# Optimization experiments

Hardware: AMD Instinct MI355X
Metric: run time of the kernel (lower is better)

The kernel has to match this reference:

```python
import jax, jax.numpy as jnp
import numpy as np

B, M = 1024, 200000
D_IN, DIM, D_OUT = 256, 128, 10
T = 1.0
EPS = 1e-7


def setup_inputs() -> dict:
    key = jax.random.key(0)
    k1, k2, k3, k4, k5 = jax.random.split(key, 5)
    x = jax.random.normal(k1, (B, D_IN), dtype=jnp.float32)
    y = jax.random.randint(k2, (B,), 0, D_OUT)
    candidate_x = jax.random.normal(k3, (M, D_IN), dtype=jnp.float32)
    candidate_y = jax.random.randint(k4, (M,), 0, D_OUT)
    W_enc = jax.random.normal(k5, (DIM, D_IN), dtype=jnp.float32) * (1.0 / np.sqrt(D_IN))
    b_enc = jnp.zeros((DIM,), dtype=jnp.float32)
    return {"x": x, "y": y, "candidate_x": candidate_x, "candidate_y": candidate_y,
            "W_enc": W_enc, "b_enc": b_enc, "is_train": 0}


def reference(x, y, candidate_x, candidate_y, W_enc, b_enc, is_train):
    # eval path (is_train == 0): no candidate subsampling, no diagonal masking
    h = x @ W_enc.T + b_enc            # [B, DIM]
    hc = candidate_x @ W_enc.T + b_enc  # [M, DIM]
    # pairwise L2 distance (cdist, p=2)
    sq = jnp.sum(h * h, axis=-1, keepdims=True) + jnp.sum(hc * hc, axis=-1)[None, :] \
         - 2.0 * (h @ hc.T)            # [B, M]
    dist = jnp.sqrt(jnp.maximum(sq, 0.0)) / T
    p = jax.nn.softmax(-dist, axis=-1)  # [B, M]
    y1h = jax.nn.one_hot(candidate_y, D_OUT, dtype=h.dtype)  # [M, D_OUT]
    logits = p @ y1h                    # [B, D_OUT]
    return jnp.log(logits + EPS)
```

## Files before the change

### kernel.cpp

```cpp
#include <hip/hip_runtime.h>
#include <hip/hip_bf16.h>
#include <math.h>

#define B_N   1024
#define M_N   200000
#define DIN   256
#define DIMN  128
#define DOUT  10
#define EPS_F 1e-7f
#define M_PAD 200064
#define NBY   1563
#define CTILES 8

typedef __bf16 bf16_t;
typedef __bf16 bf16x8 __attribute__((ext_vector_type(8)));
typedef float  f32x4  __attribute__((ext_vector_type(4)));


__global__ void cvt_w_kernel(const float* __restrict__ W, bf16_t* __restrict__ Wb){
    int i = blockIdx.x*256 + threadIdx.x;
    if (i < DIMN*DIN) Wb[i] = (bf16_t)W[i];
}

__global__ void hist_kernel(const int* __restrict__ cy, int* __restrict__ hist){
    __shared__ int h[DOUT];
    if (threadIdx.x < DOUT) h[threadIdx.x] = 0;
    __syncthreads();
    for (int i = blockIdx.x*blockDim.x + threadIdx.x; i < M_N; i += gridDim.x*blockDim.x)
        atomicAdd(&h[cy[i]], 1);
    __syncthreads();
    if (threadIdx.x < DOUT) atomicAdd(&hist[threadIdx.x*16], h[threadIdx.x]);
}

__global__ void prefix_kernel(const int* __restrict__ hist, int* __restrict__ cs){
    if (threadIdx.x == 0 && blockIdx.x == 0){
        int acc = 0;
        for (int c = 0; c < DOUT; ++c){ cs[c] = acc; acc += hist[c*16]; }
        cs[DOUT] = acc;
    }
}


__global__ __launch_bounds__(256) void encode_kernel(
    const float* __restrict__ src, const bf16_t* __restrict__ Wb,
    bf16_t* __restrict__ out, float* __restrict__ onorm, int N,
    const int* __restrict__ ycls, int* __restrict__ counters,
    const int* __restrict__ cs)
{
    __shared__ bf16_t As[128][136];
    __shared__ int   posL[128];
    __shared__ float nbuf[128][2];
    __shared__ int   cntL[DOUT], baseL[DOUT];
    const int tid = threadIdx.x;
    const int r0  = blockIdx.x*128;

    int myc = -1, myrank = 0;
    if (ycls != nullptr){
        if (tid < DOUT) cntL[tid] = 0;
        __syncthreads();
        if (tid < 128 && r0 + tid < N){
            myc = ycls[r0 + tid];
            myrank = atomicAdd(&cntL[myc], 1);
        }
        __syncthreads();
        if (tid < DOUT && cntL[tid] > 0)
            baseL[tid] = atomicAdd(&counters[tid*16], cntL[tid]);
        __syncthreads();
    }
    if (tid < 128)
        posL[tid] = (myc >= 0) ? (cs[myc] + baseL[myc] + myrank) : (r0 + tid);

    const int lane = tid & 63, wid = tid >> 6;
    const int wr = wid >> 1, wc = wid & 1;
    const int l15 = lane & 15, quad = lane >> 4;
    const int cbase = wc*64;

    f32x4 acc[4][4] = {};
    #pragma unroll
    for (int kh = 0; kh < 2; ++kh){
        __syncthreads();
        #pragma unroll
        for (int i = 0; i < 8; ++i){
            int idx = i*256 + tid;
            int row = idx >> 4;
            int col = (idx & 15)*8;
            int rr  = r0 + row; if (rr > N-1) rr = N-1;
            const float4* p4 = (const float4*)(src + (size_t)rr*DIN + kh*128 + col);
            float4 f0 = p4[0], f1 = p4[1];
            bf16x8 v;
            v[0]=(bf16_t)f0.x; v[1]=(bf16_t)f0.y; v[2]=(bf16_t)f0.z; v[3]=(bf16_t)f0.w;
            v[4]=(bf16_t)f1.x; v[5]=(bf16_t)f1.y; v[6]=(bf16_t)f1.z; v[7]=(bf16_t)f1.w;
            *(bf16x8*)&As[row][col] = v;
        }
        __syncthreads();
        #pragma unroll
        for (int ks = 0; ks < 4; ++ks){
            const int k  = ks*32 + quad*8;
            const int kg = kh*128 + k;
            bf16x8 a[4], b[4];
            #pragma unroll
            for (int rt = 0; rt < 4; ++rt)
                a[rt] = *(const bf16x8*)&As[wr*64 + rt*16 + l15][k];
            #pragma unroll
            for (int ct = 0; ct < 4; ++ct)
                b[ct] = *(const bf16x8*)(Wb + (size_t)(cbase + ct*16 + l15)*DIN + kg);
            #pragma unroll
            for (int rt = 0; rt < 4; ++rt)
                #pragma unroll
                for (int ct = 0; ct < 4; ++ct)
                    acc[rt][ct] = __builtin_amdgcn_mfma_f32_16x16x32_bf16(a[rt], b[ct], acc[rt][ct], 0, 0, 0);
        }
    }

    float np[4][4];
    #pragma unroll
    for (int rt = 0; rt < 4; ++rt)
        #pragma unroll
        for (int r = 0; r < 4; ++r){
            float s = 0.f;
            #pragma unroll
            for (int ct = 0; ct < 4; ++ct){ float v = acc[rt][ct][r]; s += v*v; }
            np[rt][r] = s;
        }
    #pragma unroll
    for (int m = 1; m < 16; m <<= 1)
        #pragma unroll
        for (int rt = 0; rt < 4; ++rt)
            #pragma unroll
            for (int r = 0; r < 4; ++r)
                np[rt][r] += __shfl_xor(np[rt][r], m, 64);
    if (l15 == 0){
        #pragma unroll
        for (int rt = 0; rt < 4; ++rt)
            #pragma unroll
            for (int r = 0; r < 4; ++r)
                nbuf[wr*64 + rt*16 + quad*4 + r][wc] = np[rt][r];
    }

    #pragma unroll
    for (int rt = 0; rt < 4; ++rt){
        #pragma unroll
        for (int r = 0; r < 4; ++r){
            int rl = wr*64 + rt*16 + quad*4 + r;
            if (r0 + rl < N){
                size_t rowp = (size_t)posL[rl]*DIMN;
                #pragma unroll
                for (int ct = 0; ct < 4; ++ct)
                    out[rowp + cbase + ct*16 + l15] = (bf16_t)acc[rt][ct][r];
            }
        }
    }
    __syncthreads();
    if (tid < 128){
        int rs = r0 + tid;
        if (rs < N) onorm[posL[tid]] = nbuf[tid][0] + nbuf[tid][1];
    }
}


__device__ __forceinline__ void bfly16(float (&s)[4][4]){
    #pragma unroll
    for (int m = 1; m < 16; m <<= 1)
        #pragma unroll
        for (int rt = 0; rt < 4; ++rt)
            #pragma unroll
            for (int r = 0; r < 4; ++r)
                s[rt][r] += __shfl_xor(s[rt][r], m, 64);
}

__device__ __forceinline__ void flushC(float (&s)[4][4], int c, int rbase,
                                       int quad, int l15, float* __restrict__ accG){
    bfly16(s);
    if (l15 == 0){
        #pragma unroll
        for (int rt = 0; rt < 4; ++rt)
            #pragma unroll
            for (int r = 0; r < 4; ++r)
                atomicAdd(&accG[(size_t)(rbase + rt*16 + quad*4 + r)*16 + c], s[rt][r]);
    }
}

__global__ __launch_bounds__(256, 2) void fused_kernel(
    const bf16_t* __restrict__ hb, const bf16_t* __restrict__ hcb,
    const float* __restrict__ hn, const float* __restrict__ hcn,
    const int* __restrict__ csg, float* __restrict__ accG)
{
    __shared__ bf16_t Bs[128][136];
    const int tid = threadIdx.x;
    const int lane = tid & 63, wid = tid >> 6;
    const int wr = wid >> 1, wc = wid & 1;
    const int l15 = lane & 15, quad = lane >> 4;
    const int rbase = blockIdx.x*128 + wr*64;

    bf16x8 a[4][4];
    #pragma unroll
    for (int ks = 0; ks < 4; ++ks)
        #pragma unroll
        for (int rt = 0; rt < 4; ++rt)
            a[ks][rt] = *(const bf16x8*)(hb + (size_t)(rbase + rt*16 + l15)*DIMN + ks*32 + quad*8);

    float hnv[4][4];
    #pragma unroll
    for (int rt = 0; rt < 4; ++rt)
        #pragma unroll
        for (int r = 0; r < 4; ++r)
            hnv[rt][r] = hn[rbase + rt*16 + quad*4 + r];

    int cseg[DOUT+1];
    #pragma unroll
    for (int i = 0; i <= DOUT; ++i) cseg[i] = csg[i];

    float s[4][4] = {};
    int curC = -1;

    for (int t = 0; t < CTILES; ++t){
        const int by = blockIdx.y*CTILES + t;
        if (by >= NBY) break;
        const int cbase0 = by*128;

        __syncthreads();
        #pragma unroll
        for (int i = 0; i < 8; ++i){
            int idx = i*256 + tid;
            int c   = idx >> 4;
            int k   = (idx & 15)*8;
            int cc  = cbase0 + c; if (cc > M_N-1) cc = M_N-1;
            *(bf16x8*)&Bs[c][k] = *(const bf16x8*)(hcb + (size_t)cc*DIMN + k);
        }
        __syncthreads();

        f32x4 acc[4][4] = {};
        #pragma unroll
        for (int ks = 0; ks < 4; ++ks){
            const int k = ks*32 + quad*8;
            bf16x8 b[4];
            #pragma unroll
            for (int ct = 0; ct < 4; ++ct)
                b[ct] = *(const bf16x8*)&Bs[wc*64 + ct*16 + l15][k];
            #pragma unroll
            for (int rt = 0; rt < 4; ++rt)
                #pragma unroll
                for (int ct = 0; ct < 4; ++ct)
                    acc[rt][ct] = __builtin_amdgcn_mfma_f32_16x16x32_bf16(a[ks][rt], b[ct], acc[rt][ct], 0, 0, 0);
        }

        float hcnv[4];
        #pragma unroll
        for (int ct = 0; ct < 4; ++ct){
            int cc = cbase0 + wc*64 + ct*16 + l15;
            hcnv[ct] = (cc < M_N) ? hcn[cc] : 1e30f;
        }
        #pragma unroll
        for (int rt = 0; rt < 4; ++rt)
            #pragma unroll
            for (int ct = 0; ct < 4; ++ct)
                #pragma unroll
                for (int r = 0; r < 4; ++r){
                    float sq = fmaxf(hnv[rt][r] + hcnv[ct] - 2.0f*acc[rt][ct][r], 0.0f);
                    acc[rt][ct][r] = __expf(-__builtin_amdgcn_sqrtf(sq));
                }

        const int lastc = min(cbase0 + 127, M_N - 1);
        int cLo = 0, cHi = 0;
        #pragma unroll
        for (int c = 1; c < DOUT; ++c){
            if (cbase0 >= cseg[c]) cLo = c;
            if (lastc  >= cseg[c]) cHi = c;
        }

        if (cLo == curC && cHi == curC){
            #pragma unroll
            for (int rt = 0; rt < 4; ++rt)
                #pragma unroll
                for (int r = 0; r < 4; ++r){
                    float v = 0.f;
                    #pragma unroll
                    for (int ct = 0; ct < 4; ++ct) v += acc[rt][ct][r];
                    s[rt][r] += v;
                }
        } else {
            if (curC >= 0) flushC(s, curC, rbase, quad, l15, accG);
            #pragma unroll
            for (int rt = 0; rt < 4; ++rt)
                #pragma unroll
                for (int r = 0; r < 4; ++r) s[rt][r] = 0.f;
            for (int c = cLo; c <= cHi; ++c){
                const int s0 = cseg[c], s1 = cseg[c+1];
                float m[4][4];
                #pragma unroll
                for (int rt = 0; rt < 4; ++rt)
                    #pragma unroll
                    for (int r = 0; r < 4; ++r){
                        float v = 0.f;
                        #pragma unroll
                        for (int ct = 0; ct < 4; ++ct){
                            int cc = cbase0 + wc*64 + ct*16 + l15;
                            v += (cc >= s0 && cc < s1) ? acc[rt][ct][r] : 0.f;
                        }
                        m[rt][r] = v;
                    }
                if (c == cHi){
                    #pragma unroll
                    for (int rt = 0; rt < 4; ++rt)
                        #pragma unroll
                        for (int r = 0; r < 4; ++r) s[rt][r] = m[rt][r];
                    curC = cHi;
                } else {
                    flushC(m, c, rbase, quad, l15, accG);
                }
            }
        }
    }
    if (curC >= 0) flushC(s, curC, rbase, quad, l15, accG);
}

__global__ void finalize_kernel(const float* __restrict__ accG, float* __restrict__ out){
    int b = blockIdx.x*blockDim.x + threadIdx.x;
    if (b < B_N){
        float v[DOUT]; float den = 0.f;
        #pragma unroll
        for (int c = 0; c < DOUT; ++c){ v[c] = accG[b*16 + c]; den += v[c]; }
        float inv = (den > 0.f) ? 1.0f/den : 0.f;
        #pragma unroll
        for (int c = 0; c < DOUT; ++c) out[b*DOUT + c] = logf(v[c]*inv + EPS_F);
    }
}


extern "C" void kernel_launch(void* const* d_in, const int* in_sizes, int n_in,
                              void* d_out, int out_size, void* d_ws, size_t ws_size,
                              hipStream_t stream)
{
    const float* x  = (const float*)d_in[0];
    const float* cx = (const float*)d_in[2];
    const int*   cy = (const int*)d_in[3];
    const float* W  = (const float*)d_in[4];
    float* out = (float*)d_out;

    char* w = (char*)d_ws;
    size_t off = 0;
    bf16_t* hcb = (bf16_t*)(w + off); off += (size_t)M_PAD*DIMN*2;
    bf16_t* hb  = (bf16_t*)(w + off); off += (size_t)B_N*DIMN*2;
    float*  hcn = (float*) (w + off); off += (size_t)M_PAD*4;
    float*  hn  = (float*) (w + off); off += (size_t)B_N*4;
    bf16_t* Wb  = (bf16_t*)(w + off); off += (size_t)DIMN*DIN*2;
    size_t zoff = off;
    float* accG = (float*)(w + off); off += (size_t)B_N*16*4;
    int* hist     = (int*)(w + off); off += 16*DOUT*4;
    int* counters = (int*)(w + off); off += 16*DOUT*4;
    int* csg      = (int*)(w + off); off += 64;
    size_t zsize = off - zoff;

    hipMemsetAsync(w + zoff, 0, zsize, stream);
    cvt_w_kernel<<<dim3((DIMN*DIN + 255)/256), dim3(256), 0, stream>>>(W, Wb);
    hist_kernel<<<dim3(256), dim3(256), 0, stream>>>(cy, hist);
    prefix_kernel<<<dim3(1), dim3(1), 0, stream>>>(hist, csg);
    encode_kernel<<<dim3(M_PAD/128), dim3(256), 0, stream>>>(cx, Wb, hcb, hcn, M_N, cy, counters, csg);
    encode_kernel<<<dim3(B_N/128), dim3(256), 0, stream>>>(x, Wb, hb, hn, B_N, nullptr, nullptr, nullptr);
    fused_kernel<<<dim3(B_N/128, (NBY + CTILES - 1)/CTILES), dim3(256), 0, stream>>>(hb, hcb, hn, hcn, csg, accG);
    finalize_kernel<<<dim3((B_N + 255)/256), dim3(256), 0, stream>>>(accG, out);
}
```

Measured before the change: 476.2 us.

## Merge prep and encode launches, prefetch encode halves, double-buffer fused tiles via LDS DMA

Merges weight conversion with the class histogram, and the candidate and query encoders, into single launches to cut launch overhead. The encoder now loads the second K-half into registers while the first half's MFMAs run. The fused distance kernel double-buffers candidate tiles in shared memory using global_load_lds direct copies with an XOR-swizzled layout, so the next tile loads while the current one computes. The launch bound of two blocks per CU is dropped and shared memory per block roughly doubles, which may lower occupancy, and the clamp on out-of-range candidate rows is removed, relying on the padded buffer.

```diff
diff --git a/kernel.cpp b/kernel.cpp
--- a/kernel.cpp
+++ b/kernel.cpp
@@ -10,23 +10,24 @@
 #define EPS_F 1e-7f
 #define M_PAD 200064
 #define NBY   1563
+#define NBX_C 1563
+#define NBX_X 8
 #define CTILES 8
+#define NGY   196
 
 typedef __bf16 bf16_t;
 typedef __bf16 bf16x8 __attribute__((ext_vector_type(8)));
 typedef float  f32x4  __attribute__((ext_vector_type(4)));
 
 
-__global__ void cvt_w_kernel(const float* __restrict__ W, bf16_t* __restrict__ Wb){
-    int i = blockIdx.x*256 + threadIdx.x;
-    if (i < DIMN*DIN) Wb[i] = (bf16_t)W[i];
-}
-
-__global__ void hist_kernel(const int* __restrict__ cy, int* __restrict__ hist){
+__global__ void prep_kernel(const float* __restrict__ W, bf16_t* __restrict__ Wb,
+                            const int* __restrict__ cy, int* __restrict__ hist){
     __shared__ int h[DOUT];
     if (threadIdx.x < DOUT) h[threadIdx.x] = 0;
     __syncthreads();
-    for (int i = blockIdx.x*blockDim.x + threadIdx.x; i < M_N; i += gridDim.x*blockDim.x)
+    int gid = blockIdx.x*256 + threadIdx.x;
+    if (gid < DIMN*DIN) Wb[gid] = (bf16_t)W[gid];
+    for (int i = gid; i < M_N; i += 256*256)
         atomicAdd(&h[cy[i]], 1);
     __syncthreads();
     if (threadIdx.x < DOUT) atomicAdd(&hist[threadIdx.x*16], h[threadIdx.x]);
@@ -42,9 +43,11 @@
 
 
 __global__ __launch_bounds__(256) void encode_kernel(
-    const float* __restrict__ src, const bf16_t* __restrict__ Wb,
-    bf16_t* __restrict__ out, float* __restrict__ onorm, int N,
-    const int* __restrict__ ycls, int* __restrict__ counters,
+    const float* __restrict__ cx, const float* __restrict__ xx,
+    const bf16_t* __restrict__ Wb,
+    bf16_t* __restrict__ hcb, bf16_t* __restrict__ hb,
+    float* __restrict__ hcn, float* __restrict__ hn,
+    const int* __restrict__ cy, int* __restrict__ counters,
     const int* __restrict__ cs)
 {
     __shared__ bf16_t As[128][136];
@@ -52,14 +55,20 @@
     __shared__ float nbuf[128][2];
     __shared__ int   cntL[DOUT], baseL[DOUT];
     const int tid = threadIdx.x;
-    const int r0  = blockIdx.x*128;
+
+    const bool isC = (blockIdx.x < NBX_C);
+    const float* __restrict__ src = isC ? cx : xx;
+    bf16_t* __restrict__ out   = isC ? hcb : hb;
+    float*  __restrict__ onorm = isC ? hcn : hn;
+    const int N  = isC ? M_N : B_N;
+    const int r0 = (isC ? blockIdx.x : blockIdx.x - NBX_C)*128;
 
     int myc = -1, myrank = 0;
-    if (ycls != nullptr){
+    if (isC){
         if (tid < DOUT) cntL[tid] = 0;
         __syncthreads();
         if (tid < 128 && r0 + tid < N){
-            myc = ycls[r0 + tid];
+            myc = cy[r0 + tid];
             myrank = atomicAdd(&cntL[myc], 1);
         }
         __syncthreads();
@@ -75,41 +84,75 @@
     const int l15 = lane & 15, quad = lane >> 4;
     const int cbase = wc*64;
 
+    float4 Rlo[8], Rhi[8];
+    #pragma unroll
+    for (int i = 0; i < 8; ++i){
+        int idx = i*256 + tid, row = idx >> 4, col = (idx & 15)*8;
+        int rr = r0 + row; if (rr > N-1) rr = N-1;
+        const float4* p4 = (const float4*)(src + (size_t)rr*DIN + col);
+        Rlo[i] = p4[0]; Rhi[i] = p4[1];
+    }
+    #pragma unroll
+    for (int i = 0; i < 8; ++i){
+        int idx = i*256 + tid, row = idx >> 4, col = (idx & 15)*8;
+        float4 f0 = Rlo[i], f1 = Rhi[i];
+        bf16x8 v;
+        v[0]=(bf16_t)f0.x; v[1]=(bf16_t)f0.y; v[2]=(bf16_t)f0.z; v[3]=(bf16_t)f0.w;
+        v[4]=(bf16_t)f1.x; v[5]=(bf16_t)f1.y; v[6]=(bf16_t)f1.z; v[7]=(bf16_t)f1.w;
+        *(bf16x8*)&As[row][col] = v;
+    }
+    __syncthreads();
+    #pragma unroll
+    for (int i = 0; i < 8; ++i){
+        int idx = i*256 + tid, row = idx >> 4, col = (idx & 15)*8;
+        int rr = r0 + row; if (rr > N-1) rr = N-1;
+        const float4* p4 = (const float4*)(src + (size_t)rr*DIN + 128 + col);
+        Rlo[i] = p4[0]; Rhi[i] = p4[1];
+    }
+
     f32x4 acc[4][4] = {};
     #pragma unroll
-    for (int kh = 0; kh < 2; ++kh){
-        __syncthreads();
-        #pragma unroll
-        for (int i = 0; i < 8; ++i){
-            int idx = i*256 + tid;
-            int row = idx >> 4;
-            int col = (idx & 15)*8;
-            int rr  = r0 + row; if (rr > N-1) rr = N-1;
-            const float4* p4 = (const float4*)(src + (size_t)rr*DIN + kh*128 + col);
-            float4 f0 = p4[0], f1 = p4[1];
-            bf16x8 v;
-            v[0]=(bf16_t)f0.x; v[1]=(bf16_t)f0.y; v[2]=(bf16_t)f0.z; v[3]=(bf16_t)f0.w;
-            v[4]=(bf16_t)f1.x; v[5]=(bf16_t)f1.y; v[6]=(bf16_t)f1.z; v[7]=(bf16_t)f1.w;
-            *(bf16x8*)&As[row][col] = v;
-        }
-        __syncthreads();
-        #pragma unroll
-        for (int ks = 0; ks < 4; ++ks){
-            const int k  = ks*32 + quad*8;
-            const int kg = kh*128 + k;
-            bf16x8 a[4], b[4];
-            #pragma unroll
-            for (int rt = 0; rt < 4; ++rt)
-                a[rt] = *(const bf16x8*)&As[wr*64 + rt*16 + l15][k];
+    for (int ks = 0; ks < 4; ++ks){
+        const int k = ks*32 + quad*8;
+        bf16x8 a[4], b[4];
+        #pragma unroll
+        for (int rt = 0; rt < 4; ++rt)
+            a[rt] = *(const bf16x8*)&As[wr*64 + rt*16 + l15][k];
+        #pragma unroll
+        for (int ct = 0; ct < 4; ++ct)
+            b[ct] = *(const bf16x8*)(Wb + (size_t)(cbase + ct*16 + l15)*DIN + k);
+        #pragma unroll
+        for (int rt = 0; rt < 4; ++rt)
             #pragma unroll
             for (int ct = 0; ct < 4; ++ct)
-                b[ct] = *(const bf16x8*)(Wb + (size_t)(cbase + ct*16 + l15)*DIN + kg);
-            #pragma unroll
-            for (int rt = 0; rt < 4; ++rt)
-                #pragma unroll
-                for (int ct = 0; ct < 4; ++ct)
-                    acc[rt][ct] = __builtin_amdgcn_mfma_f32_16x16x32_bf16(a[rt], b[ct], acc[rt][ct], 0, 0, 0);
-        }
+                acc[rt][ct] = __builtin_amdgcn_mfma_f32_16x16x32_bf16(a[rt], b[ct], acc[rt][ct], 0, 0, 0);
+    }
+    __syncthreads();
+    #pragma unroll
+    for (int i = 0; i < 8; ++i){
+        int idx = i*256 + tid, row = idx >> 4, col = (idx & 15)*8;
+        float4 f0 = Rlo[i], f1 = Rhi[i];
+        bf16x8 v;
+        v[0]=(bf16_t)f0.x; v[1]=(bf16_t)f0.y; v[2]=(bf16_t)f0.z; v[3]=(bf16_t)f0.w;
+        v[4]=(bf16_t)f1.x; v[5]=(bf16_t)f1.y; v[6]=(bf16_t)f1.z; v[7]=(bf16_t)f1.w;
+        *(bf16x8*)&As[row][col] = v;
+    }
+    __syncthreads();
+    #pragma unroll
+    for (int ks = 0; ks < 4; ++ks){
+        const int k = ks*32 + quad*8;
+        bf16x8 a[4], b[4];
+        #pragma unroll
+        for (int rt = 0; rt < 4; ++rt)
+            a[rt] = *(const bf16x8*)&As[wr*64 + rt*16 + l15][k];
+        #pragma unroll
+        for (int ct = 0; ct < 4; ++ct)
+            b[ct] = *(const bf16x8*)(Wb + (size_t)(cbase + ct*16 + l15)*DIN + 128 + k);
+        #pragma unroll
+        for (int rt = 0; rt < 4; ++rt)
+            #pragma unroll
+            for (int ct = 0; ct < 4; ++ct)
+                acc[rt][ct] = __builtin_amdgcn_mfma_f32_16x16x32_bf16(a[rt], b[ct], acc[rt][ct], 0, 0, 0);
     }
 
     float np[4][4];
@@ -180,17 +223,21 @@
     }
 }
 
-__global__ __launch_bounds__(256, 2) void fused_kernel(
+__global__ __launch_bounds__(256) void fused_kernel(
     const bf16_t* __restrict__ hb, const bf16_t* __restrict__ hcb,
     const float* __restrict__ hn, const float* __restrict__ hcn,
     const int* __restrict__ csg, float* __restrict__ accG)
 {
-    __shared__ bf16_t Bs[128][136];
+    __shared__ bf16_t Bs[2][128*DIMN];
     const int tid = threadIdx.x;
     const int lane = tid & 63, wid = tid >> 6;
     const int wr = wid >> 1, wc = wid & 1;
     const int l15 = lane & 15, quad = lane >> 4;
     const int rbase = blockIdx.x*128 + wr*64;
+    const int lrow = lane >> 4, lpos = lane & 15;
+
+    const int by0 = blockIdx.y*CTILES;
+    const int nt  = min(CTILES, NBY - by0);
 
     bf16x8 a[4][4];
     #pragma unroll
@@ -210,33 +257,41 @@
     #pragma unroll
     for (int i = 0; i <= DOUT; ++i) cseg[i] = csg[i];
 
+    auto stage = [&](int buf, int by){
+        const size_t gr0 = (size_t)by*128;
+        #pragma unroll
+        for (int j = 0; j < 8; ++j){
+            int g  = wid*8 + j;
+            int rl = g*4 + lrow;
+            int ck = lpos ^ (rl & 15);
+            const bf16_t* gp = hcb + (gr0 + rl)*DIMN + ck*8;
+            bf16_t* lp = &Bs[buf][g*512];
+            __builtin_amdgcn_global_load_lds(
+                (const __attribute__((address_space(1))) void*)gp,
+                (__attribute__((address_space(3))) void*)lp, 16, 0, 0);
+        }
+    };
+
+    stage(0, by0);
     float s[4][4] = {};
     int curC = -1;
 
-    for (int t = 0; t < CTILES; ++t){
-        const int by = blockIdx.y*CTILES + t;
-        if (by >= NBY) break;
-        const int cbase0 = by*128;
-
+    for (int t = 0; t < nt; ++t){
         __syncthreads();
-        #pragma unroll
-        for (int i = 0; i < 8; ++i){
-            int idx = i*256 + tid;
-            int c   = idx >> 4;
-            int k   = (idx & 15)*8;
-            int cc  = cbase0 + c; if (cc > M_N-1) cc = M_N-1;
-            *(bf16x8*)&Bs[c][k] = *(const bf16x8*)(hcb + (size_t)cc*DIMN + k);
-        }
-        __syncthreads();
+        if (t+1 < nt) stage((t+1)&1, by0 + t + 1);
+        const int cbase0 = (by0 + t)*128;
+        const bf16_t* bs = Bs[t&1];
 
         f32x4 acc[4][4] = {};
         #pragma unroll
         for (int ks = 0; ks < 4; ++ks){
-            const int k = ks*32 + quad*8;
             bf16x8 b[4];
             #pragma unroll
-            for (int ct = 0; ct < 4; ++ct)
-                b[ct] = *(const bf16x8*)&Bs[wc*64 + ct*16 + l15][k];
+            for (int ct = 0; ct < 4; ++ct){
+                int cand = wc*64 + ct*16 + l15;
+                int p    = (ks*4 + quad) ^ l15;
+                b[ct] = *(const bf16x8*)(bs + cand*DIMN + p*8);
+            }
             #pragma unroll
             for (int rt = 0; rt < 4; ++rt)
                 #pragma unroll
@@ -352,11 +407,9 @@
     size_t zsize = off - zoff;
 
     hipMemsetAsync(w + zoff, 0, zsize, stream);
-    cvt_w_kernel<<<dim3((DIMN*DIN + 255)/256), dim3(256), 0, stream>>>(W, Wb);
-    hist_kernel<<<dim3(256), dim3(256), 0, stream>>>(cy, hist);
+    prep_kernel<<<dim3(256), dim3(256), 0, stream>>>(W, Wb, cy, hist);
     prefix_kernel<<<dim3(1), dim3(1), 0, stream>>>(hist, csg);
-    encode_kernel<<<dim3(M_PAD/128), dim3(256), 0, stream>>>(cx, Wb, hcb, hcn, M_N, cy, counters, csg);
-    encode_kernel<<<dim3(B_N/128), dim3(256), 0, stream>>>(x, Wb, hb, hn, B_N, nullptr, nullptr, nullptr);
-    fused_kernel<<<dim3(B_N/128, (NBY + CTILES - 1)/CTILES), dim3(256), 0, stream>>>(hb, hcb, hn, hcn, csg, accG);
+    encode_kernel<<<dim3(NBX_C + NBX_X), dim3(256), 0, stream>>>(cx, x, Wb, hcb, hb, hcn, hn, cy, counters, csg);
+    fused_kernel<<<dim3(B_N/128, NGY), dim3(256), 0, stream>>>(hb, hcb, hn, hcn, csg, accG);
     finalize_kernel<<<dim3((B_N + 255)/256), dim3(256), 0, stream>>>(accG, out);
 }
```

New measurement: 517.9 us. 1.09x slower.
